# Optimization experiments

Hardware: AMD Instinct MI355X
Metric: run time of the kernel (lower is better)

The kernel has to match this reference:

```python
import jax, jax.numpy as jnp
import numpy as np

B, S, H = 64, 2048, 512
NEG_INF = -1e10


def setup_inputs() -> dict:
    key = jax.random.key(0)
    k1, k2, k3, k4, k5, k6 = jax.random.split(key, 6)
    return {
        "output": jax.random.normal(k1, (B, 1, H), dtype=jnp.float32),
        "encoder_outputs": jax.random.normal(k2, (B, S, H), dtype=jnp.float32),
        "encoder_sequence_lengths": jax.random.randint(k3, (B,), 1, S + 1, dtype=jnp.int32),
        "W1": jax.random.normal(k4, (H, H), dtype=jnp.float32) * (1.0 / np.sqrt(H)),
        "W2": jax.random.normal(k5, (H, H), dtype=jnp.float32) * (1.0 / np.sqrt(H)),
        "V": jax.random.normal(k6, (H, 1), dtype=jnp.float32) * (1.0 / np.sqrt(H)),
    }


def reference(output, encoder_outputs, encoder_sequence_lengths, W1, W2, V):
    # output: [B,1,H] decoder state (query); encoder_outputs: [B,S,H] (key & value)
    S_ = encoder_outputs.shape[1]
    key_proj = jnp.einsum('bsh,hd->bsd', encoder_outputs, W1)   # [B,S,H]
    query_proj = jnp.einsum('bqh,hd->bqd', output, W2)          # [B,1,H]
    energy = jnp.einsum('bsh,ho->bso', jnp.tanh(key_proj + query_proj), V)  # [B,S,1]
    mask = jnp.arange(S_)[None, :, None] < encoder_sequence_lengths[:, None, None]  # [B,S,1]
    energy = jnp.where(mask, energy, NEG_INF)
    attn = jax.nn.softmax(energy, axis=1)                       # [B,S,1]
    context = jnp.sum(attn * encoder_outputs, axis=1)           # [B,H]
    return context
```

## Files before the change

kernel.cpp:

```cpp
#include <hip/hip_runtime.h>
#include <hip/hip_bf16.h>

#define SS 2048
#define HH 512

typedef __attribute__((ext_vector_type(8))) short short8;
typedef __attribute__((ext_vector_type(4))) float f32x4;

__device__ __forceinline__ float bflo(unsigned u) { return __uint_as_float(u << 16); }
__device__ __forceinline__ float bfhi(unsigned u) { return __uint_as_float(u & 0xffff0000u); }

__device__ __forceinline__ short f2bf(float v) {
  __hip_bfloat16 h = __float2bfloat16(v);
  return *reinterpret_cast<short*>(&h);
}

__device__ __forceinline__ float tanh_fast(float x) {
  x = fminf(fmaxf(x, -15.f), 15.f);
  float e = __expf(2.f * x);
  return 1.f - 2.f / (e + 1.f);
}

__global__ void k_detect(const unsigned* __restrict__ Eu, int* __restrict__ flag) {
  int lane = threadIdx.x;
  unsigned w = Eu[(size_t)lane * 4097];
  unsigned e = (w >> 7) & 0xFF;
  bool inr = (e >= 90 && e <= 140);
  unsigned long long m = __ballot(inr);
  if (lane == 0) *flag = (__popcll(m) >= 48) ? 1 : 0;
}

__global__ __launch_bounds__(256) void k_transpose(const __hip_bfloat16* __restrict__ W1b,
                                                   const float* __restrict__ W1f,
                                                   const int* __restrict__ flagp,
                                                   __hip_bfloat16* __restrict__ W1T) {
  const int mode = *flagp;
  __shared__ __hip_bfloat16 t[64][65];
  int r0 = blockIdx.y * 64, c0 = blockIdx.x * 64;
  for (int i = threadIdx.x; i < 4096; i += 256) {
    int r = i >> 6, c = i & 63;
    size_t idx = (size_t)(r0 + r) * HH + c0 + c;
    float v = mode ? (float)W1b[idx] : W1f[idx];
    t[r][c] = __float2bfloat16(v);
  }
  __syncthreads();
  for (int i = threadIdx.x; i < 4096; i += 256) {
    int r = i >> 6, c = i & 63;
    W1T[(size_t)(c0 + r) * HH + r0 + c] = t[c][r];
  }
}

__global__ __launch_bounds__(256) void k_qp(const __hip_bfloat16* __restrict__ qb,
                                            const float* __restrict__ qf,
                                            const __hip_bfloat16* __restrict__ W2b,
                                            const float* __restrict__ W2f,
                                            const int* __restrict__ flagp,
                                            float* __restrict__ qp) {
  const int mode = *flagp;
  int b = blockIdx.x, h0 = blockIdx.y * 128;
  __shared__ float qs[128];
  if (threadIdx.x < 128) {
    size_t qi = (size_t)b * HH + h0 + threadIdx.x;
    qs[threadIdx.x] = mode ? (float)qb[qi] : qf[qi];
  }
  __syncthreads();
  int col = threadIdx.x * 2;
  float a0 = 0.f, a1 = 0.f;
  if (mode) {
#pragma unroll 4
    for (int i = 0; i < 128; ++i) {
      float qa = qs[i];
      unsigned u = *(const unsigned*)(W2b + (size_t)(h0 + i) * HH + col);
      a0 = fmaf(qa, bflo(u), a0);
      a1 = fmaf(qa, bfhi(u), a1);
    }
  } else {
#pragma unroll 4
    for (int i = 0; i < 128; ++i) {
      float qa = qs[i];
      float2 v = *(const float2*)(W2f + (size_t)(h0 + i) * HH + col);
      a0 = fmaf(qa, v.x, a0);
      a1 = fmaf(qa, v.y, a1);
    }
  }
  atomicAdd(&qp[b * HH + col], a0);
  atomicAdd(&qp[b * HH + col + 1], a1);
}

__global__ __launch_bounds__(256, 2) void k_energy(
    const __hip_bfloat16* __restrict__ Eb, const float* __restrict__ Ef,
    const __hip_bfloat16* __restrict__ W1T, const float* __restrict__ qp,
    const __hip_bfloat16* __restrict__ Vwb, const float* __restrict__ Vwf,
    const int* __restrict__ flagp, const int* __restrict__ lens,
    float* __restrict__ energy) {
  __shared__ __align__(16) __hip_bfloat16 Bt[128 * 32];
  __shared__ float qps[HH];
  __shared__ float Vs[HH];

  const int tid = threadIdx.x;
  const int wave = tid >> 6, lane = tid & 63;
  const int quad = lane >> 4, l16 = lane & 15;
  const int row0 = blockIdx.x * 128;
  const int b = row0 >> 11;
  if ((row0 & 2047) >= lens[b]) return;

  const int mode = *flagp;

  for (int i = tid; i < HH; i += 256) {
    qps[i] = qp[b * HH + i];
    Vs[i] = mode ? (float)Vwb[i] : Vwf[i];
  }

  short8 afr[2][16];
  {
    const size_t eBase = (size_t)row0 * HH + (size_t)(wave * 32 + l16) * HH + quad * 8;
    if (mode) {
      const __hip_bfloat16* pa = Eb + eBase;
#pragma unroll
      for (int kt = 0; kt < 16; ++kt) {
        afr[0][kt] = *(const short8*)(pa + kt * 32);
        afr[1][kt] = *(const short8*)(pa + 16 * HH + kt * 32);
      }
    } else {
      const float* pa = Ef + eBase;
#pragma unroll
      for (int kt = 0; kt < 16; ++kt) {
#pragma unroll
        for (int rb = 0; rb < 2; ++rb) {
          const float* p = pa + rb * 16 * HH + kt * 32;
          f32x4 x0 = *(const f32x4*)p;
          f32x4 x1 = *(const f32x4*)(p + 4);
          short8 v;
#pragma unroll
          for (int j = 0; j < 4; ++j) {
            v[j] = f2bf(x0[j]);
            v[j + 4] = f2bf(x1[j]);
          }
          afr[rb][kt] = v;
        }
      }
    }
  }

  const int rs0 = wave * 32 + (lane >> 2);
  const int rs1 = rs0 + 16;
  const int kg0 = ((lane & 3) - (rs0 >> 1)) & 3;
  const int kg1 = ((lane & 3) - (rs1 >> 1)) & 3;
  const __hip_bfloat16* pb0 = W1T + (size_t)rs0 * HH + kg0 * 8;
  const __hip_bfloat16* pb1 = W1T + (size_t)rs1 * HH + kg1 * 8;
  __hip_bfloat16* bW0 = Bt + wave * 1024 + lane * 8;
  __hip_bfloat16* bW1 = bW0 + 512;

  int offB[8];
#pragma unroll
  for (int cb = 0; cb < 8; ++cb) {
    int n = cb * 16 + l16;
    offB[cb] = n * 32 + (((quad + (n >> 1)) & 3) << 3);
  }

  short8 bp0 = *(const short8*)(pb0);
  short8 bp1 = *(const short8*)(pb1);

  float eacc[2][4] = {{0.f, 0.f, 0.f, 0.f}, {0.f, 0.f, 0.f, 0.f}};

  for (int nc = 0; nc < 4; ++nc) {
    f32x4 acc[2][8];
#pragma unroll
    for (int rb = 0; rb < 2; ++rb)
#pragma unroll
      for (int cb = 0; cb < 8; ++cb) acc[rb][cb] = (f32x4){0.f, 0.f, 0.f, 0.f};

#pragma unroll
    for (int kt = 0; kt < 16; ++kt) {
      __syncthreads();
      *(short8*)bW0 = bp0;
      *(short8*)bW1 = bp1;
      int t = nc * 16 + kt + 1;
      if (t > 63) t = 63;
      int o = ((t >> 4) << 16) + ((t & 15) << 5);
      bp0 = *(const short8*)(pb0 + o);
      bp1 = *(const short8*)(pb1 + o);
      __syncthreads();

      short8 af0 = afr[0][kt];
      short8 af1 = afr[1][kt];
#pragma unroll
      for (int cb = 0; cb < 8; ++cb) {
        short8 bf = *(const short8*)(Bt + offB[cb]);
        acc[0][cb] = __builtin_amdgcn_mfma_f32_16x16x32_bf16(af0, bf, acc[0][cb], 0, 0, 0);
        acc[1][cb] = __builtin_amdgcn_mfma_f32_16x16x32_bf16(af1, bf, acc[1][cb], 0, 0, 0);
      }
    }

#pragma unroll
    for (int rb = 0; rb < 2; ++rb)
#pragma unroll
      for (int cb = 0; cb < 8; ++cb) {
        int col = nc * 128 + cb * 16 + l16;
        float qv = qps[col], vv = Vs[col];
#pragma unroll
        for (int r = 0; r < 4; ++r) {
          float t = tanh_fast(acc[rb][cb][r] + qv);
          eacc[rb][r] = fmaf(vv, t, eacc[rb][r]);
        }
      }
  }

#pragma unroll
  for (int rb = 0; rb < 2; ++rb)
#pragma unroll
    for (int r = 0; r < 4; ++r) {
      float v = eacc[rb][r];
#pragma unroll
      for (int o = 1; o < 16; o <<= 1) v += __shfl_xor(v, o);
      if (l16 == 0) energy[row0 + wave * 32 + rb * 16 + quad * 4 + r] = v;
    }
}

__global__ __launch_bounds__(256) void k_stats(const float* __restrict__ energy,
                                               const int* __restrict__ lens,
                                               float* __restrict__ stats) {
  int b = blockIdx.x, tid = threadIdx.x;
  int len = lens[b];
  const float* eb = energy + b * SS;
  float m = -3.0e38f;
  for (int s = tid; s < len; s += 256) m = fmaxf(m, eb[s]);
#pragma unroll
  for (int o = 1; o < 64; o <<= 1) m = fmaxf(m, __shfl_xor(m, o));
  __shared__ float sm[4];
  __shared__ float sd[4];
  int wv = tid >> 6;
  if ((tid & 63) == 0) sm[wv] = m;
  __syncthreads();
  m = fmaxf(fmaxf(sm[0], sm[1]), fmaxf(sm[2], sm[3]));
  float ssum = 0.f;
  for (int s = tid; s < len; s += 256) ssum += __expf(eb[s] - m);
#pragma unroll
  for (int o = 1; o < 64; o <<= 1) ssum += __shfl_xor(ssum, o);
  if ((tid & 63) == 0) sd[wv] = ssum;
  __syncthreads();
  if (tid == 0) {
    stats[b * 2] = m;
    stats[b * 2 + 1] = sd[0] + sd[1] + sd[2] + sd[3];
  }
}

__global__ __launch_bounds__(256) void k_ctx(const __hip_bfloat16* __restrict__ Eb,
                                             const float* __restrict__ Ef,
                                             const float* __restrict__ energy,
                                             const float* __restrict__ stats,
                                             const int* __restrict__ lens,
                                             const int* __restrict__ flagp,
                                             float* __restrict__ ctx) {
  const int mode = *flagp;
  int bc = blockIdx.x;
  int b = bc >> 4, c = bc & 15;
  int len = lens[b];
  int s0 = c * 128;
  if (s0 >= len) return;
  int tid = threadIdx.x;
  __shared__ float p[128];
  __shared__ f32x4 part[128];
  float m = stats[b * 2];
  float inv = 1.f / stats[b * 2 + 1];
  if (tid < 128) {
    int s = s0 + tid;
    p[tid] = (s < len) ? __expf(energy[b * SS + s] - m) * inv : 0.f;
  }
  __syncthreads();
  int n = min(128, len - s0);
  int h0 = (tid & 127) * 4;
  int r = tid >> 7;
  f32x4 a = {0.f, 0.f, 0.f, 0.f};
  if (mode) {
    const __hip_bfloat16* base = Eb + (size_t)(b * SS + s0) * HH + h0;
#pragma unroll 2
    for (int i = r; i < n; i += 2) {
      float w = p[i];
      uint2 u = *(const uint2*)(base + (size_t)i * HH);
      a[0] = fmaf(w, bflo(u.x), a[0]);
      a[1] = fmaf(w, bfhi(u.x), a[1]);
      a[2] = fmaf(w, bflo(u.y), a[2]);
      a[3] = fmaf(w, bfhi(u.y), a[3]);
    }
  } else {
    const float* base = Ef + (size_t)(b * SS + s0) * HH + h0;
#pragma unroll 2
    for (int i = r; i < n; i += 2) {
      float w = p[i];
      f32x4 v = *(const f32x4*)(base + (size_t)i * HH);
      a[0] = fmaf(w, v[0], a[0]);
      a[1] = fmaf(w, v[1], a[1]);
      a[2] = fmaf(w, v[2], a[2]);
      a[3] = fmaf(w, v[3], a[3]);
    }
  }
  if (tid >= 128) part[tid - 128] = a;
  __syncthreads();
  if (tid < 128) {
    f32x4 o = part[tid];
    atomicAdd(&ctx[b * HH + h0 + 0], a[0] + o[0]);
    atomicAdd(&ctx[b * HH + h0 + 1], a[1] + o[1]);
    atomicAdd(&ctx[b * HH + h0 + 2], a[2] + o[2]);
    atomicAdd(&ctx[b * HH + h0 + 3], a[3] + o[3]);
  }
}

__global__ __launch_bounds__(256) void k_store(const float* __restrict__ ctx,
                                               const int* __restrict__ flagp,
                                               __hip_bfloat16* __restrict__ outb,
                                               float* __restrict__ outf) {
  const int mode = *flagp;
  int i = blockIdx.x * 256 + threadIdx.x;
  if (mode)
    outb[i] = __float2bfloat16(ctx[i]);
  else
    outf[i] = ctx[i];
}

extern "C" void kernel_launch(void* const* d_in, const int* in_sizes, int n_in,
                              void* d_out, int out_size, void* d_ws, size_t ws_size,
                              hipStream_t stream) {
  const __hip_bfloat16* qb  = (const __hip_bfloat16*)d_in[0];
  const float*          qf  = (const float*)d_in[0];
  const __hip_bfloat16* Eb  = (const __hip_bfloat16*)d_in[1];
  const float*          Ef  = (const float*)d_in[1];
  const int* lens           = (const int*)d_in[2];
  const __hip_bfloat16* W1b = (const __hip_bfloat16*)d_in[3];
  const float*          W1f = (const float*)d_in[3];
  const __hip_bfloat16* W2b = (const __hip_bfloat16*)d_in[4];
  const float*          W2f = (const float*)d_in[4];
  const __hip_bfloat16* Vwb = (const __hip_bfloat16*)d_in[5];
  const float*          Vwf = (const float*)d_in[5];
  __hip_bfloat16* outb      = (__hip_bfloat16*)d_out;
  float*          outf      = (float*)d_out;

  char* ws = (char*)d_ws;
  float* energy       = (float*)(ws);
  __hip_bfloat16* W1T = (__hip_bfloat16*)(ws + 524288);
  float* qp           = (float*)(ws + 1048576);
  float* ctx          = (float*)(ws + 1179648);
  float* stats        = (float*)(ws + 1310720);
  int* flag           = (int*)(ws + 1311232);

  hipMemsetAsync(ws + 1048576, 0, 262656, stream);

  k_detect<<<dim3(1), 64, 0, stream>>>((const unsigned*)d_in[1], flag);
  k_transpose<<<dim3(8, 8), 256, 0, stream>>>(W1b, W1f, flag, W1T);
  k_qp<<<dim3(64, 4), 256, 0, stream>>>(qb, qf, W2b, W2f, flag, qp);
  k_energy<<<dim3(1024), 256, 0, stream>>>(Eb, Ef, W1T, qp, Vwb, Vwf, flag, lens, energy);
  k_stats<<<dim3(64), 256, 0, stream>>>(energy, lens, stats);
  k_ctx<<<dim3(1024), 256, 0, stream>>>(Eb, Ef, energy, stats, lens, flag, ctx);
  k_store<<<dim3(128), 256, 0, stream>>>(ctx, flag, outb, outf);
}
```

Measured before the change: 483.9 us.

## Double-buffer W1 LDS tiles, fuse softmax stats into ctx, drop atomics and memset

Measured after the change: 480.9 us. Within noise of the previous version (-0.6%).

```diff
diff --git a/kernel.cpp b/kernel.cpp
--- a/kernel.cpp
+++ b/kernel.cpp
@@ -55,9 +55,9 @@
                                             const __hip_bfloat16* __restrict__ W2b,
                                             const float* __restrict__ W2f,
                                             const int* __restrict__ flagp,
-                                            float* __restrict__ qp) {
-  const int mode = *flagp;
-  int b = blockIdx.x, h0 = blockIdx.y * 128;
+                                            float* __restrict__ qp_part) {
+  const int mode = *flagp;
+  int b = blockIdx.x, p = blockIdx.y, h0 = p * 128;
   __shared__ float qs[128];
   if (threadIdx.x < 128) {
     size_t qi = (size_t)b * HH + h0 + threadIdx.x;
@@ -83,17 +83,18 @@
       a1 = fmaf(qa, v.y, a1);
     }
   }
-  atomicAdd(&qp[b * HH + col], a0);
-  atomicAdd(&qp[b * HH + col + 1], a1);
+  float* dst = qp_part + ((size_t)p * 64 + b) * HH + col;
+  dst[0] = a0;
+  dst[1] = a1;
 }
 
 __global__ __launch_bounds__(256, 2) void k_energy(
     const __hip_bfloat16* __restrict__ Eb, const float* __restrict__ Ef,
-    const __hip_bfloat16* __restrict__ W1T, const float* __restrict__ qp,
+    const __hip_bfloat16* __restrict__ W1T, const float* __restrict__ qpp,
     const __hip_bfloat16* __restrict__ Vwb, const float* __restrict__ Vwf,
     const int* __restrict__ flagp, const int* __restrict__ lens,
     float* __restrict__ energy) {
-  __shared__ __align__(16) __hip_bfloat16 Bt[128 * 32];
+  __shared__ __align__(16) __hip_bfloat16 Bt[2][128 * 32];
   __shared__ float qps[HH];
   __shared__ float Vs[HH];
 
@@ -107,7 +108,8 @@
   const int mode = *flagp;
 
   for (int i = tid; i < HH; i += 256) {
-    qps[i] = qp[b * HH + i];
+    qps[i] = qpp[(size_t)b * HH + i] + qpp[(size_t)(64 + b) * HH + i] +
+             qpp[(size_t)(128 + b) * HH + i] + qpp[(size_t)(192 + b) * HH + i];
     Vs[i] = mode ? (float)Vwb[i] : Vwf[i];
   }
 
@@ -148,8 +150,7 @@
   const int kg1 = ((lane & 3) - (rs1 >> 1)) & 3;
   const __hip_bfloat16* pb0 = W1T + (size_t)rs0 * HH + kg0 * 8;
   const __hip_bfloat16* pb1 = W1T + (size_t)rs1 * HH + kg1 * 8;
-  __hip_bfloat16* bW0 = Bt + wave * 1024 + lane * 8;
-  __hip_bfloat16* bW1 = bW0 + 512;
+  const int wslot = wave * 1024 + lane * 8;
 
   int offB[8];
 #pragma unroll
@@ -160,6 +161,11 @@
 
   short8 bp0 = *(const short8*)(pb0);
   short8 bp1 = *(const short8*)(pb1);
+  *(short8*)(&Bt[0][0] + wslot) = bp0;
+  *(short8*)(&Bt[0][0] + wslot + 512) = bp1;
+  bp0 = *(const short8*)(pb0 + 32);
+  bp1 = *(const short8*)(pb1 + 32);
+  __syncthreads();
 
   float eacc[2][4] = {{0.f, 0.f, 0.f, 0.f}, {0.f, 0.f, 0.f, 0.f}};
 
@@ -172,24 +178,30 @@
 
 #pragma unroll
     for (int kt = 0; kt < 16; ++kt) {
-      __syncthreads();
-      *(short8*)bW0 = bp0;
-      *(short8*)bW1 = bp1;
-      int t = nc * 16 + kt + 1;
-      if (t > 63) t = 63;
-      int o = ((t >> 4) << 16) + ((t & 15) << 5);
-      bp0 = *(const short8*)(pb0 + o);
-      bp1 = *(const short8*)(pb1 + o);
-      __syncthreads();
-
+      const int t = nc * 16 + kt;
+      const __hip_bfloat16* bb = &Bt[t & 1][0];
       short8 af0 = afr[0][kt];
       short8 af1 = afr[1][kt];
 #pragma unroll
       for (int cb = 0; cb < 8; ++cb) {
-        short8 bf = *(const short8*)(Bt + offB[cb]);
+        short8 bf = *(const short8*)(bb + offB[cb]);
         acc[0][cb] = __builtin_amdgcn_mfma_f32_16x16x32_bf16(af0, bf, acc[0][cb], 0, 0, 0);
         acc[1][cb] = __builtin_amdgcn_mfma_f32_16x16x32_bf16(af1, bf, acc[1][cb], 0, 0, 0);
       }
+
+      {
+        __hip_bfloat16* bw = &Bt[(t + 1) & 1][0] + wslot;
+        *(short8*)bw = bp0;
+        *(short8*)(bw + 512) = bp1;
+        int t2 = t + 2;
+        if (t2 > 63) t2 = 63;
+        int o = ((t2 >> 4) << 16) + ((t2 & 15) << 5);
+        bp0 = *(const short8*)(pb0 + o);
+        bp1 = *(const short8*)(pb1 + o);
+      }
+      asm volatile("s_waitcnt lgkmcnt(0)" ::: "memory");
+      __builtin_amdgcn_s_barrier();
+      __builtin_amdgcn_sched_barrier(0);
     }
 
 #pragma unroll
@@ -217,41 +229,12 @@
     }
 }
 
-__global__ __launch_bounds__(256) void k_stats(const float* __restrict__ energy,
-                                               const int* __restrict__ lens,
-                                               float* __restrict__ stats) {
-  int b = blockIdx.x, tid = threadIdx.x;
-  int len = lens[b];
-  const float* eb = energy + b * SS;
-  float m = -3.0e38f;
-  for (int s = tid; s < len; s += 256) m = fmaxf(m, eb[s]);
-#pragma unroll
-  for (int o = 1; o < 64; o <<= 1) m = fmaxf(m, __shfl_xor(m, o));
-  __shared__ float sm[4];
-  __shared__ float sd[4];
-  int wv = tid >> 6;
-  if ((tid & 63) == 0) sm[wv] = m;
-  __syncthreads();
-  m = fmaxf(fmaxf(sm[0], sm[1]), fmaxf(sm[2], sm[3]));
-  float ssum = 0.f;
-  for (int s = tid; s < len; s += 256) ssum += __expf(eb[s] - m);
-#pragma unroll
-  for (int o = 1; o < 64; o <<= 1) ssum += __shfl_xor(ssum, o);
-  if ((tid & 63) == 0) sd[wv] = ssum;
-  __syncthreads();
-  if (tid == 0) {
-    stats[b * 2] = m;
-    stats[b * 2 + 1] = sd[0] + sd[1] + sd[2] + sd[3];
-  }
-}
-
 __global__ __launch_bounds__(256) void k_ctx(const __hip_bfloat16* __restrict__ Eb,
                                              const float* __restrict__ Ef,
                                              const float* __restrict__ energy,
-                                             const float* __restrict__ stats,
                                              const int* __restrict__ lens,
                                              const int* __restrict__ flagp,
-                                             float* __restrict__ ctx) {
+                                             float* __restrict__ partials) {
   const int mode = *flagp;
   int bc = blockIdx.x;
   int b = bc >> 4, c = bc & 15;
@@ -259,13 +242,31 @@
   int s0 = c * 128;
   if (s0 >= len) return;
   int tid = threadIdx.x;
+  const float* eb = energy + b * SS;
+
+  float m = -3.0e38f;
+  for (int s = tid; s < len; s += 256) m = fmaxf(m, eb[s]);
+#pragma unroll
+  for (int o = 1; o < 64; o <<= 1) m = fmaxf(m, __shfl_xor(m, o));
+  __shared__ float sm[4];
+  __shared__ float sd[4];
+  int wv = tid >> 6;
+  if ((tid & 63) == 0) sm[wv] = m;
+  __syncthreads();
+  m = fmaxf(fmaxf(sm[0], sm[1]), fmaxf(sm[2], sm[3]));
+  float ssum = 0.f;
+  for (int s = tid; s < len; s += 256) ssum += __expf(eb[s] - m);
+#pragma unroll
+  for (int o = 1; o < 64; o <<= 1) ssum += __shfl_xor(ssum, o);
+  if ((tid & 63) == 0) sd[wv] = ssum;
+  __syncthreads();
+  float inv = 1.f / (sd[0] + sd[1] + sd[2] + sd[3]);
+
   __shared__ float p[128];
   __shared__ f32x4 part[128];
-  float m = stats[b * 2];
-  float inv = 1.f / stats[b * 2 + 1];
   if (tid < 128) {
     int s = s0 + tid;
-    p[tid] = (s < len) ? __expf(energy[b * SS + s] - m) * inv : 0.f;
+    p[tid] = (s < len) ? __expf(eb[s] - m) * inv : 0.f;
   }
   __syncthreads();
   int n = min(128, len - s0);
@@ -288,7 +289,7 @@
 #pragma unroll 2
     for (int i = r; i < n; i += 2) {
       float w = p[i];
-      f32x4 v = *(const f32x4*)(base + (size_t)i * HH);
+      f32x4 v = __builtin_nontemporal_load((const f32x4*)(base + (size_t)i * HH));
       a[0] = fmaf(w, v[0], a[0]);
       a[1] = fmaf(w, v[1], a[1]);
       a[2] = fmaf(w, v[2], a[2]);
@@ -299,23 +300,30 @@
   __syncthreads();
   if (tid < 128) {
     f32x4 o = part[tid];
-    atomicAdd(&ctx[b * HH + h0 + 0], a[0] + o[0]);
-    atomicAdd(&ctx[b * HH + h0 + 1], a[1] + o[1]);
-    atomicAdd(&ctx[b * HH + h0 + 2], a[2] + o[2]);
-    atomicAdd(&ctx[b * HH + h0 + 3], a[3] + o[3]);
-  }
-}
-
-__global__ __launch_bounds__(256) void k_store(const float* __restrict__ ctx,
+    f32x4 s;
+    s[0] = a[0] + o[0];
+    s[1] = a[1] + o[1];
+    s[2] = a[2] + o[2];
+    s[3] = a[3] + o[3];
+    *(f32x4*)(partials + (size_t)(b * 16 + c) * HH + h0) = s;
+  }
+}
+
+__global__ __launch_bounds__(256) void k_store(const float* __restrict__ partials,
+                                               const int* __restrict__ lens,
                                                const int* __restrict__ flagp,
                                                __hip_bfloat16* __restrict__ outb,
                                                float* __restrict__ outf) {
   const int mode = *flagp;
   int i = blockIdx.x * 256 + threadIdx.x;
+  int b = i >> 9, h = i & 511;
+  int nch = (lens[b] + 127) >> 7;
+  float s = 0.f;
+  for (int c = 0; c < nch; ++c) s += partials[(size_t)(b * 16 + c) * HH + h];
   if (mode)
-    outb[i] = __float2bfloat16(ctx[i]);
+    outb[i] = __float2bfloat16(s);
   else
-    outf[i] = ctx[i];
+    outf[i] = s;
 }
 
 extern "C" void kernel_launch(void* const* d_in, const int* in_sizes, int n_in,
@@ -338,18 +346,14 @@
   char* ws = (char*)d_ws;
   float* energy       = (float*)(ws);
   __hip_bfloat16* W1T = (__hip_bfloat16*)(ws + 524288);
-  float* qp           = (float*)(ws + 1048576);
-  float* ctx          = (float*)(ws + 1179648);
-  float* stats        = (float*)(ws + 1310720);
-  int* flag           = (int*)(ws + 1311232);
-
-  hipMemsetAsync(ws + 1048576, 0, 262656, stream);
+  float* qp_part      = (float*)(ws + 1048576);
+  float* partials     = (float*)(ws + 1572864);
+  int* flag           = (int*)(ws + 3670016);
 
   k_detect<<<dim3(1), 64, 0, stream>>>((const unsigned*)d_in[1], flag);
   k_transpose<<<dim3(8, 8), 256, 0, stream>>>(W1b, W1f, flag, W1T);
-  k_qp<<<dim3(64, 4), 256, 0, stream>>>(qb, qf, W2b, W2f, flag, qp);
-  k_energy<<<dim3(1024), 256, 0, stream>>>(Eb, Ef, W1T, qp, Vwb, Vwf, flag, lens, energy);
-  k_stats<<<dim3(64), 256, 0, stream>>>(energy, lens, stats);
-  k_ctx<<<dim3(1024), 256, 0, stream>>>(Eb, Ef, energy, stats, lens, flag, ctx);
-  k_store<<<dim3(128), 256, 0, stream>>>(ctx, flag, outb, outf);
-}
+  k_qp<<<dim3(64, 4), 256, 0, stream>>>(qb, qf, W2b, W2f, flag, qp_part);
+  k_energy<<<dim3(1024), 256, 0, stream>>>(Eb, Ef, W1T, qp_part, Vwb, Vwf, flag, lens, energy);
+  k_ctx<<<dim3(1024), 256, 0, stream>>>(Eb, Ef, energy, lens, flag, partials);
+  k_store<<<dim3(128), 256, 0, stream>>>(partials, lens, flag, outb, outf);
+}
```
